# Optimization experiments

Measured on AMD Instinct MI355X. Metric: run time of the kernel, lower is better.

## Reference

```python
import jax, jax.numpy as jnp
import numpy as np
from jax import lax

LAM = 1.0   # risk.distance calls wasserstein with lam=1
ITS = 20    # and its=20
EPS_K = 1e-6


def setup_inputs() -> dict:
    key = jax.random.key(0)
    k1, k2 = jax.random.split(key)
    N, S, D = 4096, 32, 128
    X_ls = jax.random.normal(k1, (N, S, D), dtype=jnp.float32)
    t = jax.random.randint(k2, (N,), 0, 2).astype(jnp.int32)
    return {"X_ls": X_ls, "t": t}


def _pdist2sq(X, Y):
    # squared Euclidean distance between all pairs: [nt, nc]
    C = -2.0 * (X @ Y.T)
    nx = jnp.sum(jnp.square(X), axis=1, keepdims=True)   # [nt,1]
    ny = jnp.sum(jnp.square(Y), axis=1, keepdims=True)   # [nc,1]
    return C + ny.T + nx


def _sinkhorn_step(Xt, Xc, p, lam, its):
    # Xt: [nt, d], Xc: [nc, d]  -> scalar 2*sum(T*Mt)
    nt = jnp.float32(Xt.shape[0])
    nc = jnp.float32(Xc.shape[0])
    M = _pdist2sq(Xt, Xc)                                   # [nt, nc]
    delta = lax.stop_gradient(jnp.max(M))
    eff_lam = lax.stop_gradient(lam / jnp.mean(M))
    # augmented cost matrix Mt: [nt+1, nc+1]
    row = delta * jnp.ones((1, M.shape[1]), M.dtype)
    col = jnp.concatenate([delta * jnp.ones((M.shape[0], 1), M.dtype),
                           jnp.zeros((1, 1), M.dtype)], axis=0)
    Mt = jnp.concatenate([jnp.concatenate([M, row], axis=0), col], axis=1)
    # marginals a: [nt+1,1], b: [nc+1,1]
    a = jnp.concatenate([(p / nt) * jnp.ones((Xt.shape[0], 1), M.dtype),
                         (1.0 - p) * jnp.ones((1, 1), M.dtype)], axis=0)
    b = jnp.concatenate([((1.0 - p) / nc) * jnp.ones((Xc.shape[0], 1), M.dtype),
                         p * jnp.ones((1, 1), M.dtype)], axis=0)
    K = jnp.exp(-eff_lam * Mt) + EPS_K
    ainvK = K / a
    def body(i, u):
        # u^T K -> transpose -> K^T u : [nc+1,1]
        return 1.0 / (ainvK @ (b / (K.T @ u)))
    u = lax.fori_loop(0, its, body, a)
    v = b / (K.T @ u)                                       # [nc+1,1]
    T = u * (v.T * K)                                       # [nt+1, nc+1]
    T = lax.stop_gradient(T)                                # backpropT=False
    return 2.0 * jnp.sum(T * Mt)


def _wasserstein(X_ls, t, lam=LAM, its=ITS):
    # Data-dependent split on treatment (concrete, eager) — matches tf.where+gather.
    t_np = np.asarray(t)
    it_idx = np.nonzero(t_np > 0)[0]
    ic_idx = np.nonzero(t_np < 1)[0]
    p = jnp.float32(t_np.astype(np.float32).mean())          # p_t = np.mean(t)
    Xt_all = jnp.transpose(X_ls[it_idx], (1, 0, 2))          # [S, nt, d]
    Xc_all = jnp.transpose(X_ls[ic_idx], (1, 0, 2))          # [S, nc, d]
    per_step = jax.vmap(lambda Xt, Xc: _sinkhorn_step(Xt, Xc, p, lam, its))
    return jnp.sum(per_step(Xt_all, Xc_all))                 # sum over timesteps


def reference(X_ls, t):
    return _wasserstein(X_ls, t)
```

## Files before the change

### kernel.cpp

```cpp
#include <hip/hip_runtime.h>
#include <stdint.h>

typedef unsigned char u8;
typedef unsigned short u16;
typedef uint32_t u32;

#define NTOT 4096
#define SS   32
#define DD   128
#define EPSK 1e-6f
#define NITER 20
#define CAPC 4460544u
#define LDC_FIT 2304
#define WSTR 2432
#define SU_OFF 2308
#define UNT_OFF 2309
#define BPT 16

typedef __attribute__((ext_vector_type(8))) short short8;
typedef __attribute__((ext_vector_type(4))) float f32x4;
typedef __attribute__((ext_vector_type(2))) float f32x2;

__device__ __forceinline__ float bf2f(u16 h){ return __uint_as_float(((u32)h) << 16); }
__device__ __forceinline__ u16 f2bf(float f){
  u32 u = __float_as_uint(f);
  u += 0x7fffu + ((u >> 16) & 1u);
  return (u16)(u >> 16);
}
__device__ __forceinline__ int invpermc(int cp){
  return (cp & ~63) | ((cp & 3) << 4) | ((cp >> 2) & 15);
}
__device__ __forceinline__ uint4 u4zero(){ uint4 t; t.x=0u; t.y=0u; t.z=0u; t.w=0u; return t; }

__global__ __launch_bounds__(1024) void k_compact(const int* __restrict__ t,
    int* __restrict__ itidx, int* __restrict__ icidx, int* __restrict__ meta,
    float* __restrict__ fmeta)
{
  __shared__ int sc[1024];
  int tid = threadIdx.x;
  int e0 = tid * 4;
  int tv[4]; int c = 0;
  #pragma unroll
  for (int e = 0; e < 4; e++){ tv[e] = t[e0 + e]; c += (tv[e] > 0) ? 1 : 0; }
  sc[tid] = c;
  __syncthreads();
  for (int off = 1; off < 1024; off <<= 1){
    int v = sc[tid];
    int add = (tid >= off) ? sc[tid - off] : 0;
    __syncthreads();
    sc[tid] = v + add;
    __syncthreads();
  }
  int incl = sc[tid];
  int excl = incl - c;
  int oT = excl, oC = e0 - excl;
  #pragma unroll
  for (int e = 0; e < 4; e++){
    if (tv[e] > 0) itidx[oT++] = e0 + e;
    else           icidx[oC++] = e0 + e;
  }
  if (tid == 1023){
    meta[0] = incl; meta[1] = NTOT - incl;
    fmeta[0] = (float)incl / (float)NTOT;
  }
}

__global__ void k_zero(float* __restrict__ p, int n)
{
  int i = blockIdx.x * 256 + threadIdx.x;
  if (i < n) p[i] = 0.f;
}

__global__ void k_vinit(const float* __restrict__ fmeta, float* __restrict__ w0)
{
  if (threadIdx.x == 0){
    float p = fmeta[0];
    float* w = w0 + (size_t)blockIdx.x * WSTR;
    w[SU_OFF]  = p;
    w[UNT_OFF] = 1.0f - p;
  }
}

__global__ __launch_bounds__(256) void k_pack(const float* __restrict__ X,
    const int* __restrict__ itidx, const int* __restrict__ icidx,
    const int* __restrict__ meta, u16* __restrict__ XT, u16* __restrict__ XC,
    float* __restrict__ nxT, float* __restrict__ nxC, int ts0)
{
  int r = blockIdx.x * 256 + threadIdx.x;
  int isC = blockIdx.y;
  int z = blockIdx.z;
  int s = ts0 + z;
  int n = isC ? meta[1] : meta[0];
  if (r >= n) return;
  int idx = isC ? icidx[r] : itidx[r];
  const float4* src = (const float4*)(X + ((size_t)idx * SS + s) * DD);
  u16* dst = (isC ? XC : XT) + ((size_t)z * NTOT + r) * DD;
  float nrm = 0.f;
  #pragma unroll
  for (int q = 0; q < 32; q++){
    float4 v = src[q];
    nrm += v.x*v.x + v.y*v.y + v.z*v.z + v.w*v.w;
    u32 lo = (u32)f2bf(v.x) | ((u32)f2bf(v.y) << 16);
    u32 hi = (u32)f2bf(v.z) | ((u32)f2bf(v.w) << 16);
    uint2 pk; pk.x = lo; pk.y = hi;
    ((uint2*)dst)[q] = pk;
  }
  (isC ? nxC : nxT)[z * NTOT + r] = nrm;
}

__global__ __launch_bounds__(256) void k_stats(const u16* __restrict__ XT,
    const u16* __restrict__ XC, const float* __restrict__ nxT, const float* __restrict__ nxC,
    const int* __restrict__ meta, float* __restrict__ gsx, float* __restrict__ gsn)
{
  int side = blockIdx.y, z = blockIdx.z;
  int n = side ? meta[1] : meta[0];
  int chunk = (n + 7) >> 3;
  int r0 = blockIdx.x * chunk;
  int r1 = min(r0 + chunk, n);
  const u16* B = (side ? XC : XT) + (size_t)z * NTOT * DD;
  int tid = threadIdx.x;
  int d = tid & 127, half = tid >> 7;
  float sx = 0.f;
  for (int r = r0 + half; r < r1; r += 2) sx += bf2f(B[(size_t)r * DD + d]);
  __shared__ float sp[256];
  sp[tid] = sx;
  __syncthreads();
  if (tid < 128) unsafeAtomicAdd(&gsx[(size_t)(z*2+side)*128 + tid], sp[tid] + sp[tid+128]);
  const float* nrm = (side ? nxC : nxT) + (size_t)z * NTOT;
  float sn = 0.f;
  for (int r = r0 + tid; r < r1; r += 256) sn += nrm[r];
  #pragma unroll
  for (int o = 32; o; o >>= 1) sn += __shfl_xor(sn, o);
  __syncthreads();
  if ((tid & 63) == 0) sp[tid >> 6] = sn;
  __syncthreads();
  if (tid == 0) unsafeAtomicAdd(&gsn[z*2+side], sp[0]+sp[1]+sp[2]+sp[3]);
}

__global__ void k_lam(const float* __restrict__ gsx, const float* __restrict__ gsn,
                      const int* __restrict__ meta, float* __restrict__ stats)
{
  int z = blockIdx.x, tid = threadIdx.x;
  float d = gsx[(size_t)(z*2)*128 + tid] * gsx[(size_t)(z*2+1)*128 + tid];
  #pragma unroll
  for (int o = 32; o; o >>= 1) d += __shfl_xor(d, o);
  __shared__ float rr[2];
  if ((tid & 63) == 0) rr[tid >> 6] = d;
  __syncthreads();
  if (tid == 0){
    float nt = (float)meta[0], nc = (float)meta[1];
    float msum = nc * gsn[z*2] + nt * gsn[z*2+1] - 2.f * (rr[0] + rr[1]);
    stats[z*8+0] = nt * nc / msum;
    stats[z*8+1] = msum / (nt * nc);
  }
}

#define LDA2 72
__global__ __launch_bounds__(256) void k_gemm(const u16* __restrict__ XT,
    const u16* __restrict__ XC, const float* __restrict__ nxT, const float* __restrict__ nxC,
    const int* __restrict__ meta, const float* __restrict__ fmeta,
    const float* __restrict__ stats, float* __restrict__ vmx,
    u8* __restrict__ Kc, float* __restrict__ w0base, int z0)
{
  int nt = meta[0], nc = meta[1];
  if (nt > LDC_FIT || nc > LDC_FIT) return;
  int bx = blockIdx.x, by = blockIdx.y, z = z0 + blockIdx.z;
  if (by * 128 >= nt || bx * 128 >= nc) return;
  __shared__ __align__(16) u16 As[128 * LDA2];
  __shared__ __align__(16) u16 Bs[128 * LDA2];
  __shared__ float watile[256];
  __shared__ float nxs[128];
  __shared__ float nys[128];
  __shared__ float vred[4];
  int tid = threadIdx.x;
  int wid = tid >> 6, lane = tid & 63;
  int wm = (wid >> 1) * 64, wn = (wid & 1) * 64;
  int lrow = lane & 15, lquad = lane >> 4;

  float lam = stats[z*8+0];

  if (tid < 128){
    int gi = by*128 + tid;
    nxs[tid] = (gi < nt) ? nxT[(size_t)z * NTOT + gi] : 0.f;
  } else {
    int gj = bx*128 + (tid - 128);
    nys[tid - 128] = (gj < nc) ? nxC[(size_t)z * NTOT + gj] : 0.f;
  }

  f32x4 acc[4][4];
  #pragma unroll
  for (int i = 0; i < 4; i++){
    #pragma unroll
    for (int j = 0; j < 4; j++){
      acc[i][j][0]=0.f; acc[i][j][1]=0.f; acc[i][j][2]=0.f; acc[i][j][3]=0.f;
    }
  }

  int r = tid & 127;
  int isB = tid >> 7;
  int g = (isB ? bx : by) * 128 + r;
  int lim = isB ? nc : nt;
  const u16* srcbase = (isB ? XC : XT) + ((size_t)z * NTOT + g) * DD;
  u16* dl = (isB ? Bs : As) + r * LDA2;

  auto mmstep = [&](){
    #pragma unroll
    for (int ks = 0; ks < 2; ks++){
      int koff = ks * 32 + lquad * 8;
      short8 af[4], bfr[4];
      #pragma unroll
      for (int i = 0; i < 4; i++) af[i]  = *(const short8*)(As + (wm + i*16 + lrow) * LDA2 + koff);
      #pragma unroll
      for (int j = 0; j < 4; j++) bfr[j] = *(const short8*)(Bs + (wn + j*16 + lrow) * LDA2 + koff);
      #pragma unroll
      for (int i = 0; i < 4; i++){
        #pragma unroll
        for (int j = 0; j < 4; j++){
          acc[i][j] = __builtin_amdgcn_mfma_f32_16x16x32_bf16(af[i], bfr[j], acc[i][j], 0, 0, 0);
        }
      }
    }
  };

  uint4 st[8];
  if (g < lim){
    const uint4* src = (const uint4*)(srcbase);
    #pragma unroll
    for (int q = 0; q < 8; q++) st[q] = src[q];
  } else {
    #pragma unroll
    for (int q = 0; q < 8; q++) st[q] = u4zero();
  }
  #pragma unroll
  for (int q = 0; q < 8; q++) ((uint4*)dl)[q] = st[q];
  __syncthreads();

  if (g < lim){
    const uint4* src = (const uint4*)(srcbase + 64);
    #pragma unroll
    for (int q = 0; q < 8; q++) st[q] = src[q];
  } else {
    #pragma unroll
    for (int q = 0; q < 8; q++) st[q] = u4zero();
  }

  mmstep();
  __syncthreads();
  #pragma unroll
  for (int q = 0; q < 8; q++) ((uint4*)dl)[q] = st[q];
  __syncthreads();
  mmstep();

  int ldc = (nc + 127) & ~127;
  float p = fmeta[0];
  float a0 = p / (float)nt;
  u8* Kz = Kc + (size_t)z * CAPC;

  float nyv[4]; bool jin[4];
  #pragma unroll
  for (int j = 0; j < 4; j++){
    int lcol = wn + j*16 + lrow;
    jin[j] = (bx*128 + lcol) < nc;
    nyv[j] = nys[lcol];
  }
  float vmax = 0.f;
  float colsum[4] = {0.f, 0.f, 0.f, 0.f};
  size_t cbase = (size_t)(bx*128 + wn + lrow*4);
  #pragma unroll
  for (int i = 0; i < 4; i++){
    #pragma unroll
    for (int rr2 = 0; rr2 < 4; rr2++){
      int lr = wm + i*16 + lquad*4 + rr2;
      int gi = by*128 + lr;
      bool iin = gi < nt;
      float nxv = nxs[lr];
      float cv[4];
      #pragma unroll
      for (int j = 0; j < 4; j++){
        float m = nxv + nyv[j] - 2.0f * acc[i][j][rr2];
        cv[j] = __expf(-lam * m);
        if (iin && jin[j]){ vmax = fmaxf(vmax, m); colsum[j] += cv[j]; }
      }
      u32 pk = (u32)__builtin_amdgcn_cvt_pk_fp8_f32(cv[0], cv[1], 0, false);
      pk = (u32)__builtin_amdgcn_cvt_pk_fp8_f32(cv[2], cv[3], (int)pk, true);
      if (iin) *(u32*)(Kz + (size_t)gi * ldc + cbase) = pk;
    }
  }
  #pragma unroll
  for (int j = 0; j < 4; j++){
    colsum[j] += __shfl_xor(colsum[j], 16);
    colsum[j] += __shfl_xor(colsum[j], 32);
  }
  if (lane < 16){
    #pragma unroll
    for (int j = 0; j < 4; j++) watile[wid * 64 + j*16 + lrow] = colsum[j];
  }
  #pragma unroll
  for (int o = 32; o; o >>= 1) vmax = fmaxf(vmax, __shfl_xor(vmax, o));
  if (lane == 0) vred[wid] = vmax;
  __syncthreads();
  if (tid == 0){
    float vm = fmaxf(fmaxf(vred[0], vred[1]), fmaxf(vred[2], vred[3]));
    atomicMax((int*)(vmx + (size_t)z*32), __float_as_int(vm));
  }
  if (tid < 128){
    int gj = bx*128 + tid;
    if (gj < nc){
      float v = (tid < 64) ? (watile[tid] + watile[128 + tid])
                           : (watile[64 + (tid-64)] + watile[192 + (tid-64)]);
      unsafeAtomicAdd(w0base + (size_t)z * WSTR + gj, v * a0);
    }
  }
}

__global__ __launch_bounds__(256, 2) void k_iter(const u8* __restrict__ Kc,
    const float* __restrict__ wprev, float* __restrict__ wnext,
    float* __restrict__ ubuf, const int* __restrict__ meta,
    const float* __restrict__ fmeta, const float* __restrict__ stats,
    const float* __restrict__ vmx, int writeU)
{
  __shared__ __align__(16) float zl[LDC_FIT];
  __shared__ __align__(16) float watw[4 * LDC_FIT];
  __shared__ float red[4];
  int nt = meta[0], nc = meta[1];
  if (nt > LDC_FIT || nc > LDC_FIT) return;
  int ldc = (nc + 127) & ~127;
  int z = blockIdx.y, b = blockIdx.x;
  int tid = threadIdx.x, wid = tid >> 6, lane = tid & 63;
  float p = fmeta[0];
  float b0 = (1.0f - p) / (float)nc;
  float a0 = p / (float)nt;
  float lam = stats[z*8+0];
  float delta = vmx[(size_t)z*32];
  float kc = __expf(-lam * delta);
  float kce = kc + EPSK;
  const float* wp = wprev + (size_t)z * WSTR;
  float* wnx = wnext + (size_t)z * WSTR;
  float SU = wp[SU_OFF], UNT = wp[UNT_OFF];
  float wext = EPSK * (SU + UNT) + kc * UNT;
  float wnc = kce * SU + (1.0f + EPSK) * UNT;
  float znc = p / wnc;

  float zp = 0.f;
  for (int cp = tid; cp < ldc; cp += 256){
    int c = invpermc(cp);
    float v = 0.f;
    if (c < nc) v = b0 * __builtin_amdgcn_rcpf(wp[c] + wext);
    zl[cp] = v;
    zp += v;
  }
  #pragma unroll
  for (int o = 32; o; o >>= 1) zp += __shfl_xor(zp, o);
  if (lane == 0) red[wid] = zp;
  __syncthreads();
  float Z = red[0] + red[1] + red[2] + red[3];
  float dotX = EPSK * Z + kce * znc;
  float untN = (1.0f - p) / (kce * Z + (1.0f + EPSK) * znc);

  int cb0 = lane * 16;
  float zv[48];
  #pragma unroll
  for (int s = 0; s < 3; s++){
    int cb = s*1024 + cb0;
    if (cb < ldc){
      #pragma unroll
      for (int q = 0; q < 4; q++){
        float4 t4 = *(const float4*)(zl + cb + q*4);
        zv[s*16+q*4+0]=t4.x; zv[s*16+q*4+1]=t4.y; zv[s*16+q*4+2]=t4.z; zv[s*16+q*4+3]=t4.w;
      }
    } else {
      #pragma unroll
      for (int k = 0; k < 16; k++) zv[s*16+k] = 0.f;
    }
  }

  float wacc[48];
  #pragma unroll
  for (int k = 0; k < 48; k++) wacc[k] = 0.f;
  float rsum = 0.f;

  int rpb = (nt + BPT - 1) / BPT;
  int r0 = b * rpb, r1 = min(r0 + rpb, nt);
  const u8* Kz = Kc + (size_t)z * CAPC;

  for (int r = r0 + wid; r < r1; r += 4){
    const u8* Kr = Kz + (size_t)r * ldc;
    uint4 kq[3];
    #pragma unroll
    for (int s = 0; s < 3; s++){
      int cb = s*1024 + cb0;
      if (cb < ldc) kq[s] = *(const uint4*)(Kr + cb);
      else { kq[s].x=0u; kq[s].y=0u; kq[s].z=0u; kq[s].w=0u; }
    }
    float kd[48];
    #pragma unroll
    for (int s = 0; s < 3; s++){
      u32 wd[4] = {kq[s].x, kq[s].y, kq[s].z, kq[s].w};
      #pragma unroll
      for (int q = 0; q < 4; q++){
        f32x2 d0 = __builtin_amdgcn_cvt_pk_f32_fp8((int)wd[q], false);
        f32x2 d1 = __builtin_amdgcn_cvt_pk_f32_fp8((int)wd[q], true);
        kd[s*16+q*4+0] = d0.x; kd[s*16+q*4+1] = d0.y;
        kd[s*16+q*4+2] = d1.x; kd[s*16+q*4+3] = d1.y;
      }
    }
    float d4[4] = {0.f, 0.f, 0.f, 0.f};
    #pragma unroll
    for (int k = 0; k < 48; k++) d4[k & 3] = fmaf(kd[k], zv[k], d4[k & 3]);
    float dot = (d4[0] + d4[1]) + (d4[2] + d4[3]);
    #pragma unroll
    for (int o = 32; o; o >>= 1) dot += __shfl_xor(dot, o);
    float uv = a0 * __builtin_amdgcn_rcpf(dot + dotX);
    rsum += uv;
    if (writeU && lane == 0) ubuf[(size_t)z * WSTR + r] = uv;
    #pragma unroll
    for (int k = 0; k < 48; k++) wacc[k] = fmaf(kd[k], uv, wacc[k]);
  }
  #pragma unroll
  for (int s = 0; s < 3; s++){
    int cb = s*1024 + cb0;
    if (cb < ldc){
      #pragma unroll
      for (int q = 0; q < 4; q++)
        *(float4*)(watw + (size_t)wid * LDC_FIT + cb + q*4) =
            make_float4(wacc[s*16+q*4+0], wacc[s*16+q*4+1], wacc[s*16+q*4+2], wacc[s*16+q*4+3]);
    }
  }
  if (lane == 0) unsafeAtomicAdd(wnx + SU_OFF, rsum);
  if (b == 0 && tid == 0) wnx[UNT_OFF] = untN;
  __syncthreads();
  for (int cp = tid; cp < ldc; cp += 256){
    int c = invpermc(cp);
    if (c < nc){
      float v = watw[cp] + watw[LDC_FIT + cp] + watw[2*LDC_FIT + cp] + watw[3*LDC_FIT + cp];
      unsafeAtomicAdd(wnx + c, v);
    }
  }
}

__global__ __launch_bounds__(256, 2) void k_fin(const u8* __restrict__ Kc,
    const float* __restrict__ wprev, const float* __restrict__ ubuf,
    const int* __restrict__ meta, const float* __restrict__ fmeta,
    const float* __restrict__ stats, const float* __restrict__ vmx,
    float* __restrict__ tsacc, int ts0)
{
  __shared__ __align__(16) float zl[LDC_FIT];
  __shared__ float red[4];
  int nt = meta[0], nc = meta[1];
  if (nt > LDC_FIT || nc > LDC_FIT) return;
  int ldc = (nc + 127) & ~127;
  int z = blockIdx.y, b = blockIdx.x;
  int tid = threadIdx.x, wid = tid >> 6, lane = tid & 63;
  float p = fmeta[0];
  float b0 = (1.0f - p) / (float)nc;
  float lam = stats[z*8+0];
  float invlam = stats[z*8+1];
  float delta = vmx[(size_t)z*32];
  float kc = __expf(-lam * delta);
  float kce = kc + EPSK;
  const float* wp = wprev + (size_t)z * WSTR;
  float SU = wp[SU_OFF], UNT = wp[UNT_OFF];
  float wext = EPSK * (SU + UNT) + kc * UNT;
  float wnc = kce * SU + (1.0f + EPSK) * UNT;
  float znc = p / wnc;

  float zp = 0.f;
  for (int cp = tid; cp < ldc; cp += 256){
    int c = invpermc(cp);
    float v = 0.f;
    if (c < nc) v = b0 * __builtin_amdgcn_rcpf(wp[c] + wext);
    zl[cp] = v;
    zp += v;
  }
  #pragma unroll
  for (int o = 32; o; o >>= 1) zp += __shfl_xor(zp, o);
  if (lane == 0) red[wid] = zp;
  __syncthreads();
  float Z = red[0] + red[1] + red[2] + red[3];

  int cb0 = lane * 16;
  float zv[48];
  #pragma unroll
  for (int s = 0; s < 3; s++){
    int cb = s*1024 + cb0;
    if (cb < ldc){
      #pragma unroll
      for (int q = 0; q < 4; q++){
        float4 t4 = *(const float4*)(zl + cb + q*4);
        zv[s*16+q*4+0]=t4.x; zv[s*16+q*4+1]=t4.y; zv[s*16+q*4+2]=t4.z; zv[s*16+q*4+3]=t4.w;
      }
    } else {
      #pragma unroll
      for (int k = 0; k < 16; k++) zv[s*16+k] = 0.f;
    }
  }

  int rpb = (nt + BPT - 1) / BPT;
  int r0 = b * rpb, r1 = min(r0 + rpb, nt);
  const u8* Kz = Kc + (size_t)z * CAPC;
  float wsum = 0.f;

  for (int r = r0 + wid; r < r1; r += 4){
    const u8* Kr = Kz + (size_t)r * ldc;
    float d4[4] = {0.f, 0.f, 0.f, 0.f};
    #pragma unroll
    for (int s = 0; s < 3; s++){
      int cb = s*1024 + cb0;
      if (cb < ldc){
        uint4 kq = *(const uint4*)(Kr + cb);
        u32 wd[4] = {kq.x, kq.y, kq.z, kq.w};
        #pragma unroll
        for (int q = 0; q < 4; q++){
          f32x2 d0 = __builtin_amdgcn_cvt_pk_f32_fp8((int)wd[q], false);
          f32x2 d1 = __builtin_amdgcn_cvt_pk_f32_fp8((int)wd[q], true);
          float cc[4] = {d0.x, d0.y, d1.x, d1.y};
          int k0 = s*16+q*4;
          #pragma unroll
          for (int e = 0; e < 4; e++){
            d4[e] = fmaf((cc[e] + EPSK) * zv[k0+e], __logf(fmaxf(cc[e], 1e-4f)), d4[e]);
          }
        }
      }
    }
    float inner = (d4[0] + d4[1]) + (d4[2] + d4[3]);
    #pragma unroll
    for (int o = 32; o; o >>= 1) inner += __shfl_xor(inner, o);
    wsum += ubuf[(size_t)z * WSTR + r] * inner;
  }
  if (lane == 0) unsafeAtomicAdd(tsacc + ts0 + z, -invlam * wsum);
  if (b == 0 && tid == 0){
    float aug = delta * kce * (UNT * Z + SU * znc);
    unsafeAtomicAdd(tsacc + ts0 + z, aug);
  }
}

__global__ void k_out(const float* __restrict__ tsacc, float* __restrict__ out)
{
  if (threadIdx.x == 0){
    float s = 0.f;
    for (int i = 0; i < SS; i++) s += tsacc[i];
    out[0] = 2.0f * s;
  }
}

extern "C" void kernel_launch(void* const* d_in, const int* in_sizes, int n_in,
                              void* d_out, int out_size, void* d_ws, size_t ws_size,
                              hipStream_t stream)
{
  const float* X = (const float*)d_in[0];
  const int* t = (const int*)d_in[1];

  const size_t PER_TS = 6810000u;
  const size_t FIXED  = 262144u;
  int TSG = 1;
  if (ws_size > FIXED + PER_TS){
    size_t g = (ws_size - FIXED) / PER_TS;
    TSG = (g > SS) ? SS : (int)g;
  }

  char* pp = (char*)d_ws;
  auto alloc = [&](size_t bytes) -> void* {
    void* r = (void*)pp;
    pp += (bytes + 255) & ~(size_t)255;
    return r;
  };
  u8*    Kbuf  = (u8*)alloc((size_t)TSG * CAPC);
  u16*   XT    = (u16*)alloc((size_t)TSG * NTOT * DD * 2);
  u16*   XC    = (u16*)alloc((size_t)TSG * NTOT * DD * 2);
  float* nxT   = (float*)alloc((size_t)TSG * NTOT * 4);
  float* nxC   = (float*)alloc((size_t)TSG * NTOT * 4);
  float* wbuf  = (float*)alloc((size_t)(NITER + 1) * TSG * WSTR * 4);
  float* ubuf  = (float*)alloc((size_t)TSG * WSTR * 4);
  float* auxf  = (float*)alloc((size_t)TSG * 304 * 4);
  int*   itidx = (int*)alloc(NTOT * 4);
  int*   icidx = (int*)alloc(NTOT * 4);
  int*   meta  = (int*)alloc(256);
  float* fmeta = (float*)alloc(256);
  float* tsacc = (float*)alloc(256);

  float* gsx   = auxf;
  float* gsn   = auxf + (size_t)TSG*256;
  float* stats = gsn + (size_t)TSG*2;
  float* vmx   = stats + (size_t)TSG*8;
  const int auxn = TSG * 298;
  const int wn  = (NITER + 1) * TSG * WSTR;

  k_zero<<<1, 256, 0, stream>>>(tsacc, 64);
  k_compact<<<1, 1024, 0, stream>>>(t, itidx, icidx, meta, fmeta);

  for (int ts0 = 0; ts0 < SS; ts0 += TSG){
    int cnt = SS - ts0; if (cnt > TSG) cnt = TSG;

    k_zero<<<(auxn + 255)/256, 256, 0, stream>>>(auxf, auxn);
    k_zero<<<(wn + 255)/256, 256, 0, stream>>>(wbuf, wn);
    k_vinit<<<cnt, 64, 0, stream>>>(fmeta, wbuf);
    k_pack<<<dim3(16, 2, cnt), 256, 0, stream>>>(X, itidx, icidx, meta, XT, XC, nxT, nxC, ts0);
    k_stats<<<dim3(8, 2, cnt), 256, 0, stream>>>(XT, XC, nxT, nxC, meta, gsx, gsn);
    k_lam<<<cnt, 128, 0, stream>>>(gsx, gsn, meta, stats);
    for (int zc = 0; zc < cnt; zc += 4){
      int zn = cnt - zc; if (zn > 4) zn = 4;
      k_gemm<<<dim3(18, 18, zn), 256, 0, stream>>>(XT, XC, nxT, nxC, meta, fmeta, stats, vmx, Kbuf, wbuf, zc);
    }

    for (int it = 0; it < NITER; it++){
      k_iter<<<dim3(BPT, cnt), 256, 0, stream>>>(Kbuf,
          wbuf + (size_t)it * TSG * WSTR,
          wbuf + (size_t)(it + 1) * TSG * WSTR,
          ubuf, meta, fmeta, stats, vmx, (it == NITER - 1) ? 1 : 0);
    }
    k_fin<<<dim3(BPT, cnt), 256, 0, stream>>>(Kbuf,
        wbuf + (size_t)NITER * TSG * WSTR, ubuf, meta, fmeta, stats, vmx, tsacc, ts0);
  }
  k_out<<<1, 64, 0, stream>>>(tsacc, (float*)d_out);
}
```

Baseline: 1.205 ms.

## Process two K rows per wave in iter kernel and widen finish grid

The Sinkhorn iteration kernel now has each wave handle two rows at once. It issues both rows' fp8 loads up front and interleaves their dot products and shuffle reductions, to raise memory-level parallelism and ILP. The fp8 values are decoded again for the accumulate pass instead of kept in registers, which lowers register pressure at the cost of extra converts. The finish kernel launches 64 blocks per timestep instead of 16, reduces its four waves' partials in shared memory, and does one atomic per block. Its per-timestep accumulators are spread 32 floats apart to avoid atomic contention on one cache line.

```diff
diff --git a/kernel.cpp b/kernel.cpp
--- a/kernel.cpp
+++ b/kernel.cpp
@@ -16,6 +16,7 @@
 #define SU_OFF 2308
 #define UNT_OFF 2309
 #define BPT 16
+#define BPTF 64
 
 typedef __attribute__((ext_vector_type(8))) short short8;
 typedef __attribute__((ext_vector_type(4))) float f32x4;
@@ -382,39 +383,76 @@
   int rpb = (nt + BPT - 1) / BPT;
   int r0 = b * rpb, r1 = min(r0 + rpb, nt);
   const u8* Kz = Kc + (size_t)z * CAPC;
-
-  for (int r = r0 + wid; r < r1; r += 4){
-    const u8* Kr = Kz + (size_t)r * ldc;
-    uint4 kq[3];
-    #pragma unroll
-    for (int s = 0; s < 3; s++){
-      int cb = s*1024 + cb0;
-      if (cb < ldc) kq[s] = *(const uint4*)(Kr + cb);
-      else { kq[s].x=0u; kq[s].y=0u; kq[s].z=0u; kq[s].w=0u; }
-    }
-    float kd[48];
-    #pragma unroll
-    for (int s = 0; s < 3; s++){
-      u32 wd[4] = {kq[s].x, kq[s].y, kq[s].z, kq[s].w};
-      #pragma unroll
-      for (int q = 0; q < 4; q++){
-        f32x2 d0 = __builtin_amdgcn_cvt_pk_f32_fp8((int)wd[q], false);
-        f32x2 d1 = __builtin_amdgcn_cvt_pk_f32_fp8((int)wd[q], true);
-        kd[s*16+q*4+0] = d0.x; kd[s*16+q*4+1] = d0.y;
-        kd[s*16+q*4+2] = d1.x; kd[s*16+q*4+3] = d1.y;
-      }
-    }
-    float d4[4] = {0.f, 0.f, 0.f, 0.f};
-    #pragma unroll
-    for (int k = 0; k < 48; k++) d4[k & 3] = fmaf(kd[k], zv[k], d4[k & 3]);
-    float dot = (d4[0] + d4[1]) + (d4[2] + d4[3]);
-    #pragma unroll
-    for (int o = 32; o; o >>= 1) dot += __shfl_xor(dot, o);
-    float uv = a0 * __builtin_amdgcn_rcpf(dot + dotX);
-    rsum += uv;
-    if (writeU && lane == 0) ubuf[(size_t)z * WSTR + r] = uv;
-    #pragma unroll
-    for (int k = 0; k < 48; k++) wacc[k] = fmaf(kd[k], uv, wacc[k]);
+  bool c0ok = (cb0 < ldc), c1ok = (1024 + cb0 < ldc), c2ok = (2048 + cb0 < ldc);
+
+  for (int r = r0 + wid*2; r < r1; r += 8){
+    int rB = r + 1;
+    bool bok = rB < r1;
+    const u8* KrA = Kz + (size_t)r * ldc;
+    uint4 qa0 = u4zero(), qa1 = u4zero(), qa2 = u4zero();
+    uint4 qb0 = u4zero(), qb1 = u4zero(), qb2 = u4zero();
+    if (c0ok) qa0 = *(const uint4*)(KrA + cb0);
+    if (c1ok) qa1 = *(const uint4*)(KrA + 1024 + cb0);
+    if (c2ok) qa2 = *(const uint4*)(KrA + 2048 + cb0);
+    if (bok){
+      const u8* KrB = Kz + (size_t)rB * ldc;
+      if (c0ok) qb0 = *(const uint4*)(KrB + cb0);
+      if (c1ok) qb1 = *(const uint4*)(KrB + 1024 + cb0);
+      if (c2ok) qb2 = *(const uint4*)(KrB + 2048 + cb0);
+    }
+    u32 wdA[12] = {qa0.x, qa0.y, qa0.z, qa0.w,
+                   qa1.x, qa1.y, qa1.z, qa1.w,
+                   qa2.x, qa2.y, qa2.z, qa2.w};
+    u32 wdB[12] = {qb0.x, qb0.y, qb0.z, qb0.w,
+                   qb1.x, qb1.y, qb1.z, qb1.w,
+                   qb2.x, qb2.y, qb2.z, qb2.w};
+    float d4A[4] = {0.f, 0.f, 0.f, 0.f};
+    float d4B[4] = {0.f, 0.f, 0.f, 0.f};
+    #pragma unroll
+    for (int q = 0; q < 12; q++){
+      f32x2 a0v = __builtin_amdgcn_cvt_pk_f32_fp8((int)wdA[q], false);
+      f32x2 a1v = __builtin_amdgcn_cvt_pk_f32_fp8((int)wdA[q], true);
+      d4A[0] = fmaf(a0v.x, zv[q*4+0], d4A[0]);
+      d4A[1] = fmaf(a0v.y, zv[q*4+1], d4A[1]);
+      d4A[2] = fmaf(a1v.x, zv[q*4+2], d4A[2]);
+      d4A[3] = fmaf(a1v.y, zv[q*4+3], d4A[3]);
+      f32x2 b0v = __builtin_amdgcn_cvt_pk_f32_fp8((int)wdB[q], false);
+      f32x2 b1v = __builtin_amdgcn_cvt_pk_f32_fp8((int)wdB[q], true);
+      d4B[0] = fmaf(b0v.x, zv[q*4+0], d4B[0]);
+      d4B[1] = fmaf(b0v.y, zv[q*4+1], d4B[1]);
+      d4B[2] = fmaf(b1v.x, zv[q*4+2], d4B[2]);
+      d4B[3] = fmaf(b1v.y, zv[q*4+3], d4B[3]);
+    }
+    float dotA = (d4A[0] + d4A[1]) + (d4A[2] + d4A[3]);
+    float dotB = (d4B[0] + d4B[1]) + (d4B[2] + d4B[3]);
+    #pragma unroll
+    for (int o = 32; o; o >>= 1){
+      dotA += __shfl_xor(dotA, o);
+      dotB += __shfl_xor(dotB, o);
+    }
+    float uvA = a0 * __builtin_amdgcn_rcpf(dotA + dotX);
+    float uvB = bok ? (a0 * __builtin_amdgcn_rcpf(dotB + dotX)) : 0.f;
+    rsum += uvA;
+    rsum += uvB;
+    if (writeU && lane == 0){
+      ubuf[(size_t)z * WSTR + r] = uvA;
+      if (bok) ubuf[(size_t)z * WSTR + rB] = uvB;
+    }
+    #pragma unroll
+    for (int q = 0; q < 12; q++){
+      f32x2 a0v = __builtin_amdgcn_cvt_pk_f32_fp8((int)wdA[q], false);
+      f32x2 a1v = __builtin_amdgcn_cvt_pk_f32_fp8((int)wdA[q], true);
+      wacc[q*4+0] = fmaf(a0v.x, uvA, wacc[q*4+0]);
+      wacc[q*4+1] = fmaf(a0v.y, uvA, wacc[q*4+1]);
+      wacc[q*4+2] = fmaf(a1v.x, uvA, wacc[q*4+2]);
+      wacc[q*4+3] = fmaf(a1v.y, uvA, wacc[q*4+3]);
+      f32x2 b0v = __builtin_amdgcn_cvt_pk_f32_fp8((int)wdB[q], false);
+      f32x2 b1v = __builtin_amdgcn_cvt_pk_f32_fp8((int)wdB[q], true);
+      wacc[q*4+0] = fmaf(b0v.x, uvB, wacc[q*4+0]);
+      wacc[q*4+1] = fmaf(b0v.y, uvB, wacc[q*4+1]);
+      wacc[q*4+2] = fmaf(b1v.x, uvB, wacc[q*4+2]);
+      wacc[q*4+3] = fmaf(b1v.y, uvB, wacc[q*4+3]);
+    }
   }
   #pragma unroll
   for (int s = 0; s < 3; s++){
@@ -446,6 +484,7 @@
 {
   __shared__ __align__(16) float zl[LDC_FIT];
   __shared__ float red[4];
+  __shared__ float redw[4];
   int nt = meta[0], nc = meta[1];
   if (nt > LDC_FIT || nc > LDC_FIT) return;
   int ldc = (nc + 127) & ~127;
@@ -495,7 +534,7 @@
     }
   }
 
-  int rpb = (nt + BPT - 1) / BPT;
+  int rpb = (nt + BPTF - 1) / BPTF;
   int r0 = b * rpb, r1 = min(r0 + rpb, nt);
   const u8* Kz = Kc + (size_t)z * CAPC;
   float wsum = 0.f;
@@ -527,10 +566,15 @@
     for (int o = 32; o; o >>= 1) inner += __shfl_xor(inner, o);
     wsum += ubuf[(size_t)z * WSTR + r] * inner;
   }
-  if (lane == 0) unsafeAtomicAdd(tsacc + ts0 + z, -invlam * wsum);
-  if (b == 0 && tid == 0){
-    float aug = delta * kce * (UNT * Z + SU * znc);
-    unsafeAtomicAdd(tsacc + ts0 + z, aug);
+  if (lane == 0) redw[wid] = wsum;
+  __syncthreads();
+  if (tid == 0){
+    float bs = redw[0] + redw[1] + redw[2] + redw[3];
+    float val = -invlam * bs;
+    if (b == 0){
+      val += delta * kce * (UNT * Z + SU * znc);
+    }
+    unsafeAtomicAdd(tsacc + (size_t)(ts0 + z) * 32, val);
   }
 }
 
@@ -538,7 +582,7 @@
 {
   if (threadIdx.x == 0){
     float s = 0.f;
-    for (int i = 0; i < SS; i++) s += tsacc[i];
+    for (int i = 0; i < SS; i++) s += tsacc[(size_t)i * 32];
     out[0] = 2.0f * s;
   }
 }
@@ -576,7 +620,7 @@
   int*   icidx = (int*)alloc(NTOT * 4);
   int*   meta  = (int*)alloc(256);
   float* fmeta = (float*)alloc(256);
-  float* tsacc = (float*)alloc(256);
+  float* tsacc = (float*)alloc(4096);
 
   float* gsx   = auxf;
   float* gsn   = auxf + (size_t)TSG*256;
@@ -585,7 +629,7 @@
   const int auxn = TSG * 298;
   const int wn  = (NITER + 1) * TSG * WSTR;
 
-  k_zero<<<1, 256, 0, stream>>>(tsacc, 64);
+  k_zero<<<4, 256, 0, stream>>>(tsacc, 1024);
   k_compact<<<1, 1024, 0, stream>>>(t, itidx, icidx, meta, fmeta);
 
   for (int ts0 = 0; ts0 < SS; ts0 += TSG){
@@ -608,7 +652,7 @@
           wbuf + (size_t)(it + 1) * TSG * WSTR,
           ubuf, meta, fmeta, stats, vmx, (it == NITER - 1) ? 1 : 0);
     }
-    k_fin<<<dim3(BPT, cnt), 256, 0, stream>>>(Kbuf,
+    k_fin<<<dim3(BPTF, cnt), 256, 0, stream>>>(Kbuf,
         wbuf + (size_t)NITER * TSG * WSTR, ubuf, meta, fmeta, stats, vmx, tsacc, ts0);
   }
   k_out<<<1, 64, 0, stream>>>(tsacc, (float*)d_out);
```

After: 1.114 ms. 7.5% less time.
